# Optimization experiments

Measured on AMD Instinct MI355X. Metric: run time of the kernel, lower is better.

Reference implementation:

```python
import jax, jax.numpy as jnp
import numpy as np

N = 50000   # nodes
E = 800000  # edges (avg degree 16)
IN = 256    # in_dim
H = 1       # num_heads
D = 96      # hid_dim
OUT = 128   # out_dim (LSTM hidden)


def setup_inputs() -> dict:
    key = jax.random.key(0)
    ks = jax.random.split(key, 14)
    s = 0.05
    return {
        "x": jax.random.normal(ks[0], (N, IN), jnp.float32),
        "W_fc": jax.random.normal(ks[1], (IN, H * D), jnp.float32) * s,
        "attn_l": jax.random.normal(ks[2], (H, D), jnp.float32) * s,
        "attn_r": jax.random.normal(ks[3], (H, D), jnp.float32) * s,
        "bias": jax.random.normal(ks[4], (H * D,), jnp.float32) * s,
        "W_ih": jax.random.normal(ks[5], (4 * OUT, D), jnp.float32) * s,
        "W_hh": jax.random.normal(ks[6], (4 * OUT, OUT), jnp.float32) * s,
        "b_ih": jax.random.normal(ks[7], (4 * OUT,), jnp.float32) * s,
        "b_hh": jax.random.normal(ks[8], (4 * OUT,), jnp.float32) * s,
        "h0": jax.random.normal(ks[9], (1, N, OUT), jnp.float32),
        "c0": jax.random.normal(ks[10], (1, N, OUT), jnp.float32),
        "src": jax.random.randint(ks[11], (E,), 0, N, jnp.int32),
        "dst": jax.random.randint(ks[12], (E,), 0, N, jnp.int32),
    }


def reference(x, W_fc, attn_l, attn_r, bias, W_ih, W_hh, b_ih, b_hh, h0, c0, src, dst):
    # ---- GATConv breadth step ----
    feat = (x @ W_fc).reshape(N, H, D)                       # [N,H,D]
    el = jnp.einsum("nhd,hd->nh", feat, attn_l)              # [N,H]
    er = jnp.einsum("nhd,hd->nh", feat, attn_r)              # [N,H]
    e = jax.nn.leaky_relu(el[src] + er[dst], 0.2)            # [E,H]
    # edge softmax over incoming edges of each dst node
    emax = jax.ops.segment_max(e, dst, num_segments=N)       # [N,H] (-inf if empty)
    ex = jnp.exp(e - emax[dst])                              # [E,H]
    esum = jax.ops.segment_sum(ex, dst, num_segments=N)      # [N,H]
    alpha = ex / esum[dst]                                   # [E,H]
    msg = alpha[:, :, None] * feat[src]                      # [E,H,D]
    rst = jax.ops.segment_sum(msg, dst, num_segments=N)      # [N,H,D]
    rst = rst + bias.reshape(H, D)
    # ---- tanh + mean over heads ----
    xmid = jnp.tanh(rst).mean(axis=1)                        # [N,D]
    # ---- single-step LSTM (PyTorch gate order i,f,g,o) ----
    gates = xmid @ W_ih.T + b_ih + h0[0] @ W_hh.T + b_hh     # [N,4*OUT]
    i, f, g, o = jnp.split(gates, 4, axis=-1)
    c1 = jax.nn.sigmoid(f) * c0[0] + jax.nn.sigmoid(i) * jnp.tanh(g)
    h1 = jax.nn.sigmoid(o) * jnp.tanh(c1)                    # [N,OUT]
    return h1, h1[None], c1[None]
```

## Files before the change

kernel.cpp:

```cpp
#include <hip/hip_runtime.h>
#include <math.h>

#define N_NODES 50000
#define E_EDGES 800000
#define IN_DIM  256
#define D_DIM   96
#define OUT_DIM 128
#define BKT     64
#define PREP_BLOCKS 448
#define FEAT_BLOCKS 782
#define BUCK_BLOCKS 3125
#define CAST_BLOCKS 3125

typedef __attribute__((ext_vector_type(8))) short short8;
typedef __attribute__((ext_vector_type(4))) float f32x4;

__device__ __forceinline__ unsigned short f2bf(float f) {
    unsigned u = __float_as_uint(f);
    unsigned r = u + 0x7fffu + ((u >> 16) & 1u);
    return (unsigned short)(r >> 16);
}
__device__ __forceinline__ float bf2f(unsigned short u) {
    return __uint_as_float(((unsigned)u) << 16);
}
__device__ __forceinline__ float sigm(float x) { return 1.f / (1.f + __expf(-x)); }
__device__ __forceinline__ float ftanh(float x) { return 1.f - 2.f / (1.f + __expf(2.f * x)); }

__device__ __forceinline__ int swz(int s) { return s ^ ((s >> 4) & 7); }

__device__ __forceinline__ short8 pack8(const float* __restrict__ p) {
    float4 v0 = *(const float4*)p;
    float4 v1 = *(const float4*)(p + 4);
    union { short8 s; unsigned u[4]; } r;
    r.u[0] = (unsigned)f2bf(v0.x) | ((unsigned)f2bf(v0.y) << 16);
    r.u[1] = (unsigned)f2bf(v0.z) | ((unsigned)f2bf(v0.w) << 16);
    r.u[2] = (unsigned)f2bf(v1.x) | ((unsigned)f2bf(v1.y) << 16);
    r.u[3] = (unsigned)f2bf(v1.z) | ((unsigned)f2bf(v1.w) << 16);
    return r.s;
}

__global__ __launch_bounds__(256)
void k_prep(const float* __restrict__ Wfc, const float* __restrict__ W_ih,
            const float* __restrict__ W_hh, const float* __restrict__ b_ih,
            const float* __restrict__ b_hh,
            unsigned short* __restrict__ Wfc_frag,
            unsigned short* __restrict__ Wb_frag, float* __restrict__ bsum) {
    int tid = blockIdx.x * 256 + threadIdx.x;
    if (tid < 512) bsum[tid] = b_ih[tid] + b_hh[tid];
    if (tid < 6 * 8 * 64 * 8) {
        int j = tid & 7;
        int rest = tid >> 3;
        int l = rest & 63;
        int rest2 = rest >> 6;
        int ks = rest2 & 7;
        int cf = rest2 >> 3;
        int k   = ks * 32 + (l >> 4) * 8 + j;
        int col = cf * 16 + (l & 15);
        Wfc_frag[tid] = f2bf(Wfc[k * D_DIM + col]);
    }
    if (tid < 32 * 7 * 64 * 8) {
        int j = tid & 7;
        int rest = tid >> 3;
        int l = rest & 63;
        int rest2 = rest >> 6;
        int ks = rest2 % 7;
        int cf = rest2 / 7;
        int k   = ks * 32 + (l >> 4) * 8 + j;
        int col = cf * 16 + (l & 15);
        float v = (k < 96) ? W_ih[col * 96 + k] : W_hh[col * 128 + (k - 96)];
        Wb_frag[tid] = f2bf(v);
    }
}

__global__ __launch_bounds__(256, 2)
void k_featmm_bucket_cast(const float* __restrict__ x,
                          const unsigned short* __restrict__ Wfc_frag,
                          const float* __restrict__ al, const float* __restrict__ ar,
                          unsigned short* __restrict__ feat,
                          float* __restrict__ el, float* __restrict__ er,
                          const int* __restrict__ src, const int* __restrict__ dst,
                          int* __restrict__ cnt, unsigned short* __restrict__ ebuf16,
                          const float* __restrict__ h0, unsigned short* __restrict__ h0b) {
    if (blockIdx.x >= FEAT_BLOCKS) {
        int seg = blockIdx.x - FEAT_BLOCKS;
        if (seg < BUCK_BLOCKS) {
            int e = seg * 256 + threadIdx.x;
            if (e < E_EDGES) {
                int d = dst[e];
                int pos = atomicAdd(&cnt[d], 1);
                ebuf16[(size_t)d * BKT + pos] = (unsigned short)src[e];
            }
        } else {
            int tid = (seg - BUCK_BLOCKS) * 256 + threadIdx.x;
            if (tid < N_NODES * OUT_DIM / 8)
                *(short8*)(h0b + (size_t)tid * 8) = pack8(h0 + (size_t)tid * 8);
        }
        return;
    }
    const int t     = threadIdx.x;
    const int lane  = t & 63;
    const int w     = t >> 6;
    const int nfrag = lane & 15;
    const int khalf = lane >> 4;
    const int node  = blockIdx.x * 64 + w * 16 + nfrag;
    const int r     = min(node, N_NODES - 1);

    f32x4 acc[6];
#pragma unroll
    for (int cf = 0; cf < 6; ++cf) acc[cf] = (f32x4){0.f, 0.f, 0.f, 0.f};

    const float* px = x + (size_t)r * IN_DIM + khalf * 8;
    const unsigned short* pW = Wfc_frag + (size_t)lane * 8;

#pragma unroll 1
    for (int ks = 0; ks < 8; ++ks) {
        short8 xf = pack8(px + ks * 32);
#pragma unroll
        for (int cf = 0; cf < 6; ++cf) {
            short8 wf = *(const short8*)(pW + (size_t)((cf * 8 + ks) * 64) * 8);
            acc[cf] = __builtin_amdgcn_mfma_f32_16x16x32_bf16(wf, xf, acc[cf], 0, 0, 0);
        }
    }

    float sl = 0.f, sr = 0.f;
#pragma unroll
    for (int cf = 0; cf < 6; ++cf) {
        const int oc = cf * 16 + khalf * 4;
        const float4 a = *(const float4*)(al + oc);
        const float4 b = *(const float4*)(ar + oc);
        sl += acc[cf][0]*a.x + acc[cf][1]*a.y + acc[cf][2]*a.z + acc[cf][3]*a.w;
        sr += acc[cf][0]*b.x + acc[cf][1]*b.y + acc[cf][2]*b.z + acc[cf][3]*b.w;
    }
    sl += __shfl_xor(sl, 16, 64); sl += __shfl_xor(sl, 32, 64);
    sr += __shfl_xor(sr, 16, 64); sr += __shfl_xor(sr, 32, 64);

    if (node < N_NODES) {
        if (lane < 16) { el[node] = sl; er[node] = sr; }
#pragma unroll
        for (int cf = 0; cf < 6; ++cf) {
            const int oc = cf * 16 + khalf * 4;
            union { unsigned u[2]; } pk;
            pk.u[0] = (unsigned)f2bf(acc[cf][0]) | ((unsigned)f2bf(acc[cf][1]) << 16);
            pk.u[1] = (unsigned)f2bf(acc[cf][2]) | ((unsigned)f2bf(acc[cf][3]) << 16);
            *(uint2*)(feat + (size_t)node * D_DIM + oc) = make_uint2(pk.u[0], pk.u[1]);
        }
    }
}

__global__ __launch_bounds__(256)
void k_gather(const int* __restrict__ cnt, const unsigned short* __restrict__ ebuf16,
              const float* __restrict__ el, const float* __restrict__ er,
              const unsigned short* __restrict__ feat, const float* __restrict__ bias,
              unsigned short* __restrict__ xmid) {
    const int n    = (blockIdx.x * 256 + threadIdx.x) >> 5;
    const int lane = threadIdx.x & 31;
    if (n >= N_NODES) return;
    const size_t o0 = (size_t)n * BKT;
    const int deg = cnt[n];
    const float ern = er[n];

    float a0 = 0.f, a1 = 0.f, a2 = 0.f;
    float inv;

    if (deg <= 32) {
        int   s_l = 0;
        float v_l = -INFINITY;
        if (lane < deg) {
            s_l = ebuf16[o0 + lane];
            float v = el[s_l] + ern; v_l = v > 0.f ? v : 0.2f * v;
        }
        float vmax = v_l;
#pragma unroll
        for (int d = 16; d; d >>= 1) vmax = fmaxf(vmax, __shfl_xor(vmax, d, 32));
        float w_l = (lane < deg) ? __expf(v_l - vmax) : 0.f;
        float ssum = w_l;
#pragma unroll
        for (int d = 16; d; d >>= 1) ssum += __shfl_xor(ssum, d, 32);
        inv = 1.f / (ssum > 0.f ? ssum : 1.f);

        for (int i = 0; i < deg; ++i) {
            int   s = __shfl(s_l, i, 32);
            float w = __shfl(w_l, i, 32);
            const unsigned short* fr = feat + (size_t)s * D_DIM;
            a0 += w * bf2f(fr[lane]);
            a1 += w * bf2f(fr[lane + 32]);
            a2 += w * bf2f(fr[lane + 64]);
        }
    } else {
        float vmax = -INFINITY;
        for (int i = lane; i < deg; i += 32) {
            int s = ebuf16[o0 + i];
            float v = el[s] + ern; v = v > 0.f ? v : 0.2f * v;
            vmax = fmaxf(vmax, v);
        }
#pragma unroll
        for (int d = 16; d; d >>= 1) vmax = fmaxf(vmax, __shfl_xor(vmax, d, 32));

        float ssum = 0.f;
        for (int i = lane; i < deg; i += 32) {
            int s = ebuf16[o0 + i];
            float v = el[s] + ern; v = v > 0.f ? v : 0.2f * v;
            ssum += __expf(v - vmax);
        }
#pragma unroll
        for (int d = 16; d; d >>= 1) ssum += __shfl_xor(ssum, d, 32);
        inv = 1.f / (ssum > 0.f ? ssum : 1.f);

        for (int bi0 = 0; bi0 < deg; bi0 += 32) {
            int   i_l = bi0 + lane;
            int   s_l = 0; float w_l = 0.f;
            if (i_l < deg) {
                s_l = ebuf16[o0 + i_l];
                float v = el[s_l] + ern; v = v > 0.f ? v : 0.2f * v;
                w_l = __expf(v - vmax);
            }
            int m = min(32, deg - bi0);
            for (int i = 0; i < m; ++i) {
                int   s = __shfl(s_l, i, 32);
                float w = __shfl(w_l, i, 32);
                const unsigned short* fr = feat + (size_t)s * D_DIM;
                a0 += w * bf2f(fr[lane]);
                a1 += w * bf2f(fr[lane + 32]);
                a2 += w * bf2f(fr[lane + 64]);
            }
        }
    }

    unsigned short* zr = xmid + (size_t)n * D_DIM;
    zr[lane]      = f2bf(ftanh(a0 * inv + bias[lane]));
    zr[lane + 32] = f2bf(ftanh(a1 * inv + bias[lane + 32]));
    zr[lane + 64] = f2bf(ftanh(a2 * inv + bias[lane + 64]));
}

__global__ __launch_bounds__(256, 6)
void k_lstm_mfma(const unsigned short* __restrict__ xmid,
                 const unsigned short* __restrict__ h0b,
                 const unsigned short* __restrict__ Wb_frag,
                 const float* __restrict__ bsum,
                 const float* __restrict__ cin0,
                 float* __restrict__ out_h1a, float* __restrict__ out_h1b,
                 float* __restrict__ out_c1) {
    __shared__ unsigned short lds_a[7 * 64 * 8];
    __shared__ float lds_c[16][132];
    const int t     = threadIdx.x;
    const int lane  = t & 63;
    const int w     = t >> 6;
    const int n0    = blockIdx.x * 16;
    const int nfrag = lane & 15;
    const int khalf = lane >> 4;
    const int node  = n0 + nfrag;

    if (t < 192) {
        int rr = t / 12;
        int ch = t % 12;
        short8 v = *(const short8*)(xmid + (size_t)(n0 + rr) * D_DIM + ch * 8);
        int s = (ch >> 2) * 64 + (ch & 3) * 16 + rr;
        *(short8*)(lds_a + (size_t)swz(s) * 8) = v;
    }
    {
        int rr = t >> 4;
        int ch = t & 15;
        short8 v = *(const short8*)(h0b + (size_t)(n0 + rr) * OUT_DIM + ch * 8);
        int s = (3 + (ch >> 2)) * 64 + (ch & 3) * 16 + rr;
        *(short8*)(lds_a + (size_t)swz(s) * 8) = v;
    }
    {
        int rr = t >> 4;
        int cc0 = (t & 15) * 8;
        float4 a = *(const float4*)(cin0 + (size_t)(n0 + rr) * OUT_DIM + cc0);
        float4 b = *(const float4*)(cin0 + (size_t)(n0 + rr) * OUT_DIM + cc0 + 4);
        *(float4*)(&lds_c[rr][cc0])     = a;
        *(float4*)(&lds_c[rr][cc0 + 4]) = b;
    }
    __syncthreads();

    f32x4 acc[2][4];
#pragma unroll
    for (int cc = 0; cc < 2; ++cc)
#pragma unroll
        for (int g = 0; g < 4; ++g)
            acc[cc][g] = (f32x4){0.f, 0.f, 0.f, 0.f};

    const unsigned short* pW = Wb_frag + (size_t)lane * 8;

#pragma unroll
    for (int ks = 0; ks < 7; ++ks) {
        short8 zf = *(const short8*)(lds_a + (size_t)swz(ks * 64 + lane) * 8);
        short8 wf[4][2];
#pragma unroll
        for (int g = 0; g < 4; ++g)
#pragma unroll
            for (int cc = 0; cc < 2; ++cc) {
                int cf = w * 2 + cc + 8 * g;
                wf[g][cc] = *(const short8*)(pW + (size_t)(cf * 7 + ks) * 512);
            }
#pragma unroll
        for (int g = 0; g < 4; ++g)
#pragma unroll
            for (int cc = 0; cc < 2; ++cc)
                acc[cc][g] = __builtin_amdgcn_mfma_f32_16x16x32_bf16(
                    wf[g][cc], zf, acc[cc][g], 0, 0, 0);
    }

#pragma unroll
    for (int cc = 0; cc < 2; ++cc) {
        const int oc = (w * 2 + cc) * 16 + khalf * 4;
        const float4 bi = *(const float4*)(bsum + oc);
        const float4 bf = *(const float4*)(bsum + 128 + oc);
        const float4 bg = *(const float4*)(bsum + 256 + oc);
        const float4 bo = *(const float4*)(bsum + 384 + oc);
        const f32x4 I = acc[cc][0];
        const f32x4 F = acc[cc][1];
        const f32x4 G = acc[cc][2];
        const f32x4 O = acc[cc][3];
        const float4 cv = *(const float4*)(&lds_c[nfrag][oc]);
        float4 h1, c1;
        c1.x = sigm(F[0] + bf.x) * cv.x + sigm(I[0] + bi.x) * ftanh(G[0] + bg.x);
        c1.y = sigm(F[1] + bf.y) * cv.y + sigm(I[1] + bi.y) * ftanh(G[1] + bg.y);
        c1.z = sigm(F[2] + bf.z) * cv.z + sigm(I[2] + bi.z) * ftanh(G[2] + bg.z);
        c1.w = sigm(F[3] + bf.w) * cv.w + sigm(I[3] + bi.w) * ftanh(G[3] + bg.w);
        h1.x = sigm(O[0] + bo.x) * ftanh(c1.x);
        h1.y = sigm(O[1] + bo.y) * ftanh(c1.y);
        h1.z = sigm(O[2] + bo.z) * ftanh(c1.z);
        h1.w = sigm(O[3] + bo.w) * ftanh(c1.w);
        *(float4*)(out_h1a + (size_t)node * OUT_DIM + oc) = h1;
        *(float4*)(out_h1b + (size_t)node * OUT_DIM + oc) = h1;
        *(float4*)(out_c1  + (size_t)node * OUT_DIM + oc) = c1;
    }
}

extern "C" void kernel_launch(void* const* d_in, const int* in_sizes, int n_in,
                              void* d_out, int out_size, void* d_ws, size_t ws_size,
                              hipStream_t stream) {
    const float* x      = (const float*)d_in[0];
    const float* W_fc   = (const float*)d_in[1];
    const float* attn_l = (const float*)d_in[2];
    const float* attn_r = (const float*)d_in[3];
    const float* bias   = (const float*)d_in[4];
    const float* W_ih   = (const float*)d_in[5];
    const float* W_hh   = (const float*)d_in[6];
    const float* b_ih   = (const float*)d_in[7];
    const float* b_hh   = (const float*)d_in[8];
    const float* h0     = (const float*)d_in[9];
    const float* c0     = (const float*)d_in[10];
    const int*   src    = (const int*)d_in[11];
    const int*   dst    = (const int*)d_in[12];
    float* out = (float*)d_out;

    char* base = (char*)d_ws;
    unsigned short* feat     = (unsigned short*)(base);
    unsigned short* xmid     = (unsigned short*)(base + 9600000);
    unsigned short* h0b      = (unsigned short*)(base + 19200000);
    float*          el       = (float*)(base + 32000000);
    float*          er       = (float*)(base + 32200000);
    int*            cnt      = (int*)(base + 32400000);
    unsigned short* ebuf16   = (unsigned short*)(base + 32600000);
    unsigned short* Wb_frag  = (unsigned short*)(base + 39000000);
    float*          bsum     = (float*)(base + 39229376);
    unsigned short* Wfc_frag = (unsigned short*)(base + 39231424);

    hipMemsetAsync(cnt, 0, (size_t)N_NODES * sizeof(int), stream);

    k_prep<<<PREP_BLOCKS, 256, 0, stream>>>(W_fc, W_ih, W_hh, b_ih, b_hh,
                                            Wfc_frag, Wb_frag, bsum);

    k_featmm_bucket_cast<<<FEAT_BLOCKS + BUCK_BLOCKS + CAST_BLOCKS, 256, 0, stream>>>(
        x, Wfc_frag, attn_l, attn_r, feat, el, er, src, dst, cnt, ebuf16, h0, h0b);

    k_gather<<<(N_NODES * 32 + 255) / 256, 256, 0, stream>>>(cnt, ebuf16, el, er,
                                                             feat, bias, xmid);

    k_lstm_mfma<<<(N_NODES + 15) / 16, 256, 0, stream>>>(xmid, h0b, Wb_frag, bsum, c0,
                                                         out, out + N_NODES * OUT_DIM,
                                                         out + 2 * N_NODES * OUT_DIM);
}
```

Before: 162.1 us.

## Make LSTM kernel persistent with LDS-resident weight half and double-buffered tiles

Replaces the one-block-per-16-node LSTM kernel with a persistent kernel of 256 blocks. Each block keeps half of the gate weights (64 output columns) resident in LDS and loops over node tiles, double-buffering the bf16 input tiles through registers into LDS. The goal is to stop re-reading the weight fragments from global memory for every tile and to overlap loading the next tile with the current MFMA work. The cost is that only 256 workgroups run at one per CU with large LDS, so occupancy is lower. Each input tile is also loaded twice, once by each column-half block.

New measurement: 156.6 us. 3.4% less time.

```diff
diff --git a/kernel.cpp b/kernel.cpp
--- a/kernel.cpp
+++ b/kernel.cpp
@@ -11,6 +11,7 @@
 #define FEAT_BLOCKS 782
 #define BUCK_BLOCKS 3125
 #define CAST_BLOCKS 3125
+#define NTILES      3125
 
 typedef __attribute__((ext_vector_type(8))) short short8;
 typedef __attribute__((ext_vector_type(4))) float f32x4;
@@ -232,100 +233,117 @@
     zr[lane + 64] = f2bf(ftanh(a2 * inv + bias[lane + 64]));
 }
 
-__global__ __launch_bounds__(256, 6)
-void k_lstm_mfma(const unsigned short* __restrict__ xmid,
-                 const unsigned short* __restrict__ h0b,
-                 const unsigned short* __restrict__ Wb_frag,
-                 const float* __restrict__ bsum,
-                 const float* __restrict__ cin0,
-                 float* __restrict__ out_h1a, float* __restrict__ out_h1b,
-                 float* __restrict__ out_c1) {
-    __shared__ unsigned short lds_a[7 * 64 * 8];
-    __shared__ float lds_c[16][132];
+__global__ __launch_bounds__(256, 1)
+void k_lstm_persist(const unsigned short* __restrict__ xmid,
+                    const unsigned short* __restrict__ h0b,
+                    const unsigned short* __restrict__ Wb_frag,
+                    const float* __restrict__ bsum,
+                    const float* __restrict__ cin0,
+                    float* __restrict__ out_h1a, float* __restrict__ out_h1b,
+                    float* __restrict__ out_c1) {
+    __shared__ unsigned short wlds[16 * 7 * 64 * 8];
+    __shared__ unsigned short alds[2][7 * 64 * 8];
     const int t     = threadIdx.x;
     const int lane  = t & 63;
-    const int w     = t >> 6;
-    const int n0    = blockIdx.x * 16;
+    const int wv    = t >> 6;
     const int nfrag = lane & 15;
     const int khalf = lane >> 4;
-    const int node  = n0 + nfrag;
-
-    if (t < 192) {
-        int rr = t / 12;
-        int ch = t % 12;
-        short8 v = *(const short8*)(xmid + (size_t)(n0 + rr) * D_DIM + ch * 8);
-        int s = (ch >> 2) * 64 + (ch & 3) * 16 + rr;
-        *(short8*)(lds_a + (size_t)swz(s) * 8) = v;
-    }
+    const int ch    = blockIdx.x >> 7;
+    const int b7    = blockIdx.x & 127;
+
+#pragma unroll 4
+    for (int it = 0; it < 28; ++it) {
+        int cidx = t + it * 256;
+        int wg   = cidx / 448;
+        int rem  = cidx % 448;
+        int cf   = ch * 4 + (wg >> 2) + 8 * (wg & 3);
+        *(short8*)(wlds + (size_t)cidx * 8) =
+            *(const short8*)(Wb_frag + ((size_t)cf * 448 + rem) * 8);
+    }
+
+    const int oc = ch * 64 + wv * 16 + khalf * 4;
+    const float4 bi = *(const float4*)(bsum + oc);
+    const float4 bf = *(const float4*)(bsum + 128 + oc);
+    const float4 bg = *(const float4*)(bsum + 256 + oc);
+    const float4 bo = *(const float4*)(bsum + 384 + oc);
+
+    const int U = (NTILES - b7 + 127) / 128;
+
+    short8 r0, r1;
+    int s0 = 0, s1 = 0;
     {
-        int rr = t >> 4;
-        int ch = t & 15;
-        short8 v = *(const short8*)(h0b + (size_t)(n0 + rr) * OUT_DIM + ch * 8);
-        int s = (3 + (ch >> 2)) * 64 + (ch & 3) * 16 + rr;
-        *(short8*)(lds_a + (size_t)swz(s) * 8) = v;
-    }
-    {
-        int rr = t >> 4;
-        int cc0 = (t & 15) * 8;
-        float4 a = *(const float4*)(cin0 + (size_t)(n0 + rr) * OUT_DIM + cc0);
-        float4 b = *(const float4*)(cin0 + (size_t)(n0 + rr) * OUT_DIM + cc0 + 4);
-        *(float4*)(&lds_c[rr][cc0])     = a;
-        *(float4*)(&lds_c[rr][cc0 + 4]) = b;
-    }
+        int tile = b7, n0 = tile * 16;
+        { int q = t;
+          if (q < 192) { int rr = q / 12, ck = q % 12;
+              r0 = *(const short8*)(xmid + (size_t)(n0 + rr) * D_DIM + ck * 8);
+              s0 = (ck >> 2) * 64 + (ck & 3) * 16 + rr;
+          } else { int p = q - 192; int rr = p >> 4, ck = p & 15;
+              r0 = *(const short8*)(h0b + (size_t)(n0 + rr) * OUT_DIM + ck * 8);
+              s0 = (3 + (ck >> 2)) * 64 + (ck & 3) * 16 + rr; } }
+        if (t < 192) { int p = t + 64;
+            int rr = p >> 4, ck = p & 15;
+            r1 = *(const short8*)(h0b + (size_t)(n0 + rr) * OUT_DIM + ck * 8);
+            s1 = (3 + (ck >> 2)) * 64 + (ck & 3) * 16 + rr; }
+    }
+    *(short8*)(alds[0] + (size_t)swz(s0) * 8) = r0;
+    if (t < 192) *(short8*)(alds[0] + (size_t)swz(s1) * 8) = r1;
     __syncthreads();
 
-    f32x4 acc[2][4];
-#pragma unroll
-    for (int cc = 0; cc < 2; ++cc)
-#pragma unroll
-        for (int g = 0; g < 4; ++g)
-            acc[cc][g] = (f32x4){0.f, 0.f, 0.f, 0.f};
-
-    const unsigned short* pW = Wb_frag + (size_t)lane * 8;
-
-#pragma unroll
-    for (int ks = 0; ks < 7; ++ks) {
-        short8 zf = *(const short8*)(lds_a + (size_t)swz(ks * 64 + lane) * 8);
-        short8 wf[4][2];
-#pragma unroll
-        for (int g = 0; g < 4; ++g)
-#pragma unroll
-            for (int cc = 0; cc < 2; ++cc) {
-                int cf = w * 2 + cc + 8 * g;
-                wf[g][cc] = *(const short8*)(pW + (size_t)(cf * 7 + ks) * 512);
+    for (int u = 0; u < U; ++u) {
+        const int cur  = u & 1;
+        const int tile = b7 + u * 128;
+        const int n0   = tile * 16;
+        const int node = n0 + nfrag;
+
+        if (u + 1 < U) {
+            int nn0 = (tile + 128) * 16;
+            { int q = t;
+              if (q < 192) { int rr = q / 12, ck = q % 12;
+                  r0 = *(const short8*)(xmid + (size_t)(nn0 + rr) * D_DIM + ck * 8);
+              } else { int p = q - 192; int rr = p >> 4, ck = p & 15;
+                  r0 = *(const short8*)(h0b + (size_t)(nn0 + rr) * OUT_DIM + ck * 8); } }
+            if (t < 192) { int p = t + 64;
+                int rr = p >> 4, ck = p & 15;
+                r1 = *(const short8*)(h0b + (size_t)(nn0 + rr) * OUT_DIM + ck * 8); }
+        }
+
+        const float4 cv = *(const float4*)(cin0 + (size_t)node * OUT_DIM + oc);
+
+        f32x4 acc[4];
+#pragma unroll
+        for (int g = 0; g < 4; ++g) acc[g] = (f32x4){0.f, 0.f, 0.f, 0.f};
+
+#pragma unroll
+        for (int ks = 0; ks < 7; ++ks) {
+            short8 zf = *(const short8*)(alds[cur] + (size_t)swz(ks * 64 + lane) * 8);
+#pragma unroll
+            for (int g = 0; g < 4; ++g) {
+                short8 wf = *(const short8*)(wlds +
+                    (size_t)(((wv * 4 + g) * 7 + ks) * 64 + lane) * 8);
+                acc[g] = __builtin_amdgcn_mfma_f32_16x16x32_bf16(wf, zf, acc[g], 0, 0, 0);
             }
-#pragma unroll
-        for (int g = 0; g < 4; ++g)
-#pragma unroll
-            for (int cc = 0; cc < 2; ++cc)
-                acc[cc][g] = __builtin_amdgcn_mfma_f32_16x16x32_bf16(
-                    wf[g][cc], zf, acc[cc][g], 0, 0, 0);
-    }
-
-#pragma unroll
-    for (int cc = 0; cc < 2; ++cc) {
-        const int oc = (w * 2 + cc) * 16 + khalf * 4;
-        const float4 bi = *(const float4*)(bsum + oc);
-        const float4 bf = *(const float4*)(bsum + 128 + oc);
-        const float4 bg = *(const float4*)(bsum + 256 + oc);
-        const float4 bo = *(const float4*)(bsum + 384 + oc);
-        const f32x4 I = acc[cc][0];
-        const f32x4 F = acc[cc][1];
-        const f32x4 G = acc[cc][2];
-        const f32x4 O = acc[cc][3];
-        const float4 cv = *(const float4*)(&lds_c[nfrag][oc]);
-        float4 h1, c1;
-        c1.x = sigm(F[0] + bf.x) * cv.x + sigm(I[0] + bi.x) * ftanh(G[0] + bg.x);
-        c1.y = sigm(F[1] + bf.y) * cv.y + sigm(I[1] + bi.y) * ftanh(G[1] + bg.y);
-        c1.z = sigm(F[2] + bf.z) * cv.z + sigm(I[2] + bi.z) * ftanh(G[2] + bg.z);
-        c1.w = sigm(F[3] + bf.w) * cv.w + sigm(I[3] + bi.w) * ftanh(G[3] + bg.w);
-        h1.x = sigm(O[0] + bo.x) * ftanh(c1.x);
-        h1.y = sigm(O[1] + bo.y) * ftanh(c1.y);
-        h1.z = sigm(O[2] + bo.z) * ftanh(c1.z);
-        h1.w = sigm(O[3] + bo.w) * ftanh(c1.w);
-        *(float4*)(out_h1a + (size_t)node * OUT_DIM + oc) = h1;
-        *(float4*)(out_h1b + (size_t)node * OUT_DIM + oc) = h1;
-        *(float4*)(out_c1  + (size_t)node * OUT_DIM + oc) = c1;
+        }
+
+        {
+            float4 h1, c1;
+            c1.x = sigm(acc[1][0] + bf.x) * cv.x + sigm(acc[0][0] + bi.x) * ftanh(acc[2][0] + bg.x);
+            c1.y = sigm(acc[1][1] + bf.y) * cv.y + sigm(acc[0][1] + bi.y) * ftanh(acc[2][1] + bg.y);
+            c1.z = sigm(acc[1][2] + bf.z) * cv.z + sigm(acc[0][2] + bi.z) * ftanh(acc[2][2] + bg.z);
+            c1.w = sigm(acc[1][3] + bf.w) * cv.w + sigm(acc[0][3] + bi.w) * ftanh(acc[2][3] + bg.w);
+            h1.x = sigm(acc[3][0] + bo.x) * ftanh(c1.x);
+            h1.y = sigm(acc[3][1] + bo.y) * ftanh(c1.y);
+            h1.z = sigm(acc[3][2] + bo.z) * ftanh(c1.z);
+            h1.w = sigm(acc[3][3] + bo.w) * ftanh(c1.w);
+            *(float4*)(out_h1a + (size_t)node * OUT_DIM + oc) = h1;
+            *(float4*)(out_h1b + (size_t)node * OUT_DIM + oc) = h1;
+            *(float4*)(out_c1  + (size_t)node * OUT_DIM + oc) = c1;
+        }
+
+        if (u + 1 < U) {
+            *(short8*)(alds[cur ^ 1] + (size_t)swz(s0) * 8) = r0;
+            if (t < 192) *(short8*)(alds[cur ^ 1] + (size_t)swz(s1) * 8) = r1;
+        }
+        __syncthreads();
     }
 }
 
@@ -370,7 +388,7 @@
     k_gather<<<(N_NODES * 32 + 255) / 256, 256, 0, stream>>>(cnt, ebuf16, el, er,
                                                              feat, bias, xmid);
 
-    k_lstm_mfma<<<(N_NODES + 15) / 16, 256, 0, stream>>>(xmid, h0b, Wb_frag, bsum, c0,
-                                                         out, out + N_NODES * OUT_DIM,
-                                                         out + 2 * N_NODES * OUT_DIM);
-}
+    k_lstm_persist<<<256, 256, 0, stream>>>(xmid, h0b, Wb_frag, bsum, c0,
+                                            out, out + N_NODES * OUT_DIM,
+                                            out + 2 * N_NODES * OUT_DIM);
+}
```
